# Optimization experiments

Measured on AMD Instinct MI355X. Metric: run time of the kernel, lower is better.

Reference implementation:

```python
import jax, jax.numpy as jnp
import numpy as np

E = 128          # embedding_dim
H = 128          # decoder_hidden_dim
N = 200000       # number of candidate nodes


def setup_inputs() -> dict:
    key = jax.random.key(0)
    k0, k1, k2, k3, k4, k5 = jax.random.split(key, 6)
    return {
        "current_node_emb": jax.random.normal(k0, (1, E), jnp.float32),
        "context_emb": jax.random.normal(k1, (1, E), jnp.float32),
        "candidate_node_embs": jax.random.normal(k2, (N, E), jnp.float32),
        "Wq": jax.random.normal(k3, (H, 2 * E), jnp.float32) * 0.05,  # nn.Linear(2E->H, bias=False) weight
        "Wk": jax.random.normal(k4, (H, E), jnp.float32) * 0.05,      # nn.Linear(E->H, bias=False) weight
        "mask": jax.random.randint(k5, (1, N), 0, 2, jnp.int32),
    }


def reference(current_node_emb, context_emb, candidate_node_embs, Wq, Wk, mask):
    # combined_input = cat([current, context], dim=1) -> [1, 2E]
    combined = jnp.concatenate([current_node_emb, context_emb], axis=1)
    query = combined @ Wq.T                      # [1, H]
    keys = candidate_node_embs @ Wk.T            # [N, H]
    attn_scores = query @ keys.T                 # [1, N]
    masked = jnp.where(mask == 0, -jnp.inf, attn_scores)
    probs = jax.nn.softmax(masked, axis=1)       # [1, N]

    n = probs.shape[1]
    k = min(50, max(1, int(0.5 * n)))            # static Python int -> jit-friendly
    top_probs, _ = jax.lax.top_k(probs, k)       # [1, k]
    threshold = top_probs[:, -1:]                # [1, 1]
    top_mask = probs >= threshold
    filtered = probs * top_mask
    filtered = filtered / (jnp.sum(filtered, axis=1, keepdims=True) + 1e-10)

    log_probs_all = jnp.log(filtered + 1e-10)    # [1, N]
    # Categorical(filtered): true-zero probability outside top-k
    logits = jnp.where(filtered > 0, jnp.log(filtered), -jnp.inf)
    action_idx = jax.random.categorical(jax.random.key(42), logits, axis=1)  # [1]
    log_prob_action = jnp.take_along_axis(logits, action_idx[:, None], axis=1)[:, 0]  # [1]
    return (log_probs_all, log_prob_action, action_idx)
```

## Files before the change

### kernel.cpp

```cpp
#include <hip/hip_runtime.h>
#include <math.h>


#define CAP 4096
#define NEG_INF (-__builtin_inff())

__device__ __forceinline__ unsigned int f2ord(float f){
  unsigned int b = __float_as_uint(f);
  return (b & 0x80000000u) ? ~b : (b | 0x80000000u);
}
__device__ __forceinline__ unsigned int rotl32(unsigned int x, int d){
  return (x << d) | (x >> (32 - d));
}

__device__ float gumbel_from_idx(unsigned int idx){
  unsigned int x0 = 0u, x1 = idx;
  const unsigned int ks0 = 0u, ks1 = 42u;
  const unsigned int ks2 = 0u ^ 42u ^ 0x1BD11BDAu;
  x0 += ks0; x1 += ks1;
#define TF_RND(r) { x0 += x1; x1 = rotl32(x1, (r)); x1 ^= x0; }
  TF_RND(13) TF_RND(15) TF_RND(26) TF_RND(6)
  x0 += ks1; x1 += ks2 + 1u;
  TF_RND(17) TF_RND(29) TF_RND(16) TF_RND(24)
  x0 += ks2; x1 += ks0 + 2u;
  TF_RND(13) TF_RND(15) TF_RND(26) TF_RND(6)
  x0 += ks0; x1 += ks1 + 3u;
  TF_RND(17) TF_RND(29) TF_RND(16) TF_RND(24)
  x0 += ks1; x1 += ks2 + 4u;
  TF_RND(13) TF_RND(15) TF_RND(26) TF_RND(6)
  x0 += ks2; x1 += ks0 + 5u;
#undef TF_RND
  unsigned int bits = x0 ^ x1;
  unsigned int fb = (bits >> 9) | 0x3f800000u;
  float f = __uint_as_float(fb) - 1.0f;
  float u = (f < 1.17549435e-38f) ? 1.17549435e-38f : f;
  return -logf(-logf(u));
}

__global__ void k_prep(const float* __restrict__ cur, const float* __restrict__ ctx,
                       const float* __restrict__ Wq, const float* __restrict__ Wk,
                       float* __restrict__ v, unsigned int* __restrict__ hist,
                       unsigned int* __restrict__ scal_u){
  __shared__ float comb[256];
  __shared__ float q[128];
  int t = threadIdx.x;
  for (int k = t; k < 2048; k += 256) hist[k] = 0u;
  if (t < 16) scal_u[t] = 0u;
  comb[t] = (t < 128) ? cur[t] : ctx[t - 128];
  __syncthreads();
  if (t < 128){
    float acc = 0.f;
    const float* row = Wq + t * 256;
    for (int j = 0; j < 256; ++j) acc = fmaf(row[j], comb[j], acc);
    q[t] = acc;
  }
  __syncthreads();
  if (t < 128){
    float acc = 0.f;
    for (int h = 0; h < 128; ++h) acc = fmaf(q[h], Wk[h * 128 + t], acc);
    v[t] = acc;
  }
}

__global__ __launch_bounds__(256) void k_score(const float* __restrict__ cand,
    const int* __restrict__ mask, const float* __restrict__ v,
    float* __restrict__ scores, float* __restrict__ out, int N){
  const float NLOG = logf(1e-10f);
  int t = threadIdx.x;
  int lane = t & 63, wave = t >> 6;
  int hi = lane >> 5, hl = lane & 31;
  float4 v4 = ((const float4*)v)[hl];
  const float4* cp = (const float4*)cand;
  int base = (blockIdx.x * 4 + wave) * 16;
  float4 c[8];
  #pragma unroll
  for (int k = 0; k < 8; ++k){
    int r = base + 2 * k + hi;
    r = (r < N) ? r : (N - 1);
    c[k] = cp[(size_t)r * 32 + hl];
  }
  float p[8];
  #pragma unroll
  for (int k = 0; k < 8; ++k)
    p[k] = fmaf(c[k].x, v4.x, fmaf(c[k].y, v4.y, fmaf(c[k].z, v4.z, c[k].w * v4.w)));
  #pragma unroll
  for (int k = 0; k < 8; ++k){
    p[k] += __shfl_xor(p[k], 1, 64);
    p[k] += __shfl_xor(p[k], 2, 64);
    p[k] += __shfl_xor(p[k], 4, 64);
    p[k] += __shfl_xor(p[k], 8, 64);
    p[k] += __shfl_xor(p[k], 16, 64);
  }
  float sv = p[0];
  #pragma unroll
  for (int k = 1; k < 8; ++k) sv = (hl == k) ? p[k] : sv;
  if (hl < 8){
    int r = base + 2 * hl + hi;
    if (r < N) scores[r] = mask[r] ? sv : NEG_INF;
  }
  int rr = blockIdx.x * 64 + t;
  if (t < 64 && rr < N) out[rr] = NLOG;
}

__global__ __launch_bounds__(256) void k_hist(const float* __restrict__ scores,
    unsigned int* __restrict__ hist, unsigned int* __restrict__ scal_u,
    int N, int ktop){
  __shared__ unsigned int lhist[2048];
  __shared__ float wsum[4];
  __shared__ int is_last;
  int t = threadIdx.x;
  int lane = t & 63, wave = t >> 6;
  for (int k = t; k < 2048; k += 256) lhist[k] = 0u;
  __syncthreads();
  float ez = 0.f;
  int i0 = (blockIdx.x * 256 + t) * 4;
  if (i0 + 3 < N){
    float4 s4 = *(const float4*)(scores + i0);
    float ss[4] = {s4.x, s4.y, s4.z, s4.w};
    #pragma unroll
    for (int e = 0; e < 4; ++e){
      if (ss[e] > NEG_INF){
        atomicAdd(&lhist[f2ord(ss[e]) >> 21], 1u);
        ez += expf(ss[e]);
      }
    }
  } else {
    for (int e = 0; e < 4; ++e){
      int i = i0 + e;
      if (i < N){
        float s = scores[i];
        if (s > NEG_INF){ atomicAdd(&lhist[f2ord(s) >> 21], 1u); ez += expf(s); }
      }
    }
  }
  #pragma unroll
  for (int off = 32; off; off >>= 1) ez += __shfl_xor(ez, off, 64);
  if (lane == 0) wsum[wave] = ez;
  __syncthreads();
  for (int k = t; k < 2048; k += 256){
    unsigned int c = lhist[k];
    if (c) atomicAdd(&hist[k], c);
  }
  if (t == 0) atomicAdd((float*)scal_u + 3, wsum[0] + wsum[1] + wsum[2] + wsum[3]);
  __syncthreads();
  if (t == 0){
    __threadfence();
    unsigned int old = atomicAdd(&scal_u[6], 1u);
    is_last = (old == gridDim.x - 1u);
  }
  __syncthreads();
  if (!is_last) return;
  __threadfence();
  __shared__ unsigned int suf[256];
  __shared__ int csel_sh;
  unsigned int csum = 0;
  for (int k = 0; k < 8; ++k) csum += hist[t * 8 + k];
  suf[t] = csum;
  if (t == 0) csel_sh = -1;
  __syncthreads();
  for (int d = 1; d < 256; d <<= 1){
    unsigned int add = (t + d < 256) ? suf[t + d] : 0u;
    __syncthreads();
    suf[t] += add;
    __syncthreads();
  }
  unsigned int st = suf[t];
  unsigned int sn = (t < 255) ? suf[t + 1] : 0u;
  if (st >= (unsigned)ktop && sn < (unsigned)ktop) csel_sh = t;
  __syncthreads();
  if (t == 0){
    int b_sel = 0;
    if (csel_sh >= 0){
      int c = csel_sh;
      unsigned int cum = (c < 255) ? suf[c + 1] : 0u;
      for (int b = 8 * c + 7; b >= 8 * c; --b){
        cum += hist[b];
        if (cum >= (unsigned)ktop){ b_sel = b; break; }
      }
    }
    scal_u[1] = ((unsigned int)b_sel) << 21;
  }
}

__global__ __launch_bounds__(256) void k_gather(const float* __restrict__ scores,
    unsigned int* __restrict__ scal_u, unsigned int* __restrict__ buf_idx,
    float* __restrict__ buf_s, float* __restrict__ out, int N, int ktop){
  int t = threadIdx.x;
  unsigned int u_lo = scal_u[1];
  int i0 = (blockIdx.x * 256 + t) * 4;
  if (i0 + 3 < N){
    float4 s4 = *(const float4*)(scores + i0);
    float ss[4] = {s4.x, s4.y, s4.z, s4.w};
    #pragma unroll
    for (int e = 0; e < 4; ++e){
      float s = ss[e];
      if (s > NEG_INF && f2ord(s) >= u_lo){
        unsigned int pos = atomicAdd(&scal_u[0], 1u);
        if (pos < CAP){ buf_idx[pos] = (unsigned int)(i0 + e); buf_s[pos] = s; }
      }
    }
  } else {
    for (int e = 0; e < 4; ++e){
      int i = i0 + e;
      if (i < N){
        float s = scores[i];
        if (s > NEG_INF && f2ord(s) >= u_lo){
          unsigned int pos = atomicAdd(&scal_u[0], 1u);
          if (pos < CAP){ buf_idx[pos] = (unsigned int)i; buf_s[pos] = s; }
        }
      }
    }
  }
  __syncthreads();
  __shared__ int is_last;
  if (t == 0){
    __threadfence();
    unsigned int old = atomicAdd(&scal_u[7], 1u);
    is_last = (old == gridDim.x - 1u);
  }
  __syncthreads();
  if (!is_last) return;
  __threadfence();
  float* scal_f = (float*)scal_u;
  __shared__ float s_lds[CAP];
  __shared__ float thr_sh;
  __shared__ float wred[4];
  __shared__ float rv[4], rl[4];
  __shared__ unsigned int ri[4];
  int C = (int)scal_u[0]; if (C > CAP) C = CAP;
  for (int j = t; j < C; j += 256) s_lds[j] = buf_s[j];
  if (t == 0) thr_sh = NEG_INF;
  __syncthreads();
  if (C > ktop){
    for (int j = t; j < C; j += 256){
      float sj = s_lds[j];
      int g = 0, e = 0;
      for (int k2 = 0; k2 < C; ++k2){
        float sk = s_lds[k2];
        g += (sk > sj);
        e += (sk == sj);
      }
      if (g < ktop && g + e >= ktop) thr_sh = sj;
    }
  }
  __syncthreads();
  float s_thr = thr_sh;
  float Z = scal_f[3];
  float part = 0.f;
  for (int j = t; j < C; j += 256){
    float sj = s_lds[j];
    if (sj >= s_thr) part += expf(sj);
  }
  #pragma unroll
  for (int off = 32; off; off >>= 1) part += __shfl_xor(part, off, 64);
  int wave = t >> 6, lane = t & 63;
  if (lane == 0) wred[wave] = part;
  __syncthreads();
  float T = wred[0] + wred[1] + wred[2] + wred[3];
  float D = T + 1e-10f * Z;
  float lnD = logf(D);
  for (int j = t; j < C; j += 256){
    float sj = s_lds[j];
    if (sj >= s_thr) out[buf_idx[j]] = logf(expf(sj - lnD) + 1e-10f);
  }
  float bestv = NEG_INF, bestlogit = NEG_INF;
  unsigned int bestidx = 0xFFFFFFFFu;
  for (int j = t; j < C; j += 256){
    float sj = s_lds[j];
    if (sj >= s_thr){
      unsigned int idx = buf_idx[j];
      float logit = sj - lnD;
      float val = logit + gumbel_from_idx(idx);
      if (val > bestv || (val == bestv && idx < bestidx)){
        bestv = val; bestlogit = logit; bestidx = idx;
      }
    }
  }
  #pragma unroll
  for (int off = 32; off; off >>= 1){
    float ov = __shfl_xor(bestv, off, 64);
    float ol = __shfl_xor(bestlogit, off, 64);
    unsigned int oi = (unsigned int)__shfl_xor((int)bestidx, off, 64);
    if (ov > bestv || (ov == bestv && oi < bestidx)){
      bestv = ov; bestlogit = ol; bestidx = oi;
    }
  }
  if (lane == 0){ rv[wave] = bestv; rl[wave] = bestlogit; ri[wave] = bestidx; }
  __syncthreads();
  if (t == 0){
    for (int w = 1; w < 4; ++w){
      if (rv[w] > rv[0] || (rv[w] == rv[0] && ri[w] < ri[0])){
        rv[0] = rv[w]; rl[0] = rl[w]; ri[0] = ri[w];
      }
    }
    out[N] = rl[0];
    out[N + 1] = (float)ri[0];
  }
}

extern "C" void kernel_launch(void* const* d_in, const int* in_sizes, int n_in,
                              void* d_out, int out_size, void* d_ws, size_t ws_size,
                              hipStream_t stream){
  const float* cur  = (const float*)d_in[0];
  const float* ctx  = (const float*)d_in[1];
  const float* cand = (const float*)d_in[2];
  const float* Wq   = (const float*)d_in[3];
  const float* Wk   = (const float*)d_in[4];
  const int*   mask = (const int*)d_in[5];
  int N = in_sizes[5];
  float* out = (float*)d_out;

  char* ws = (char*)d_ws;
  unsigned int* scal_u  = (unsigned int*)ws;
  unsigned int* hist    = (unsigned int*)(ws + 256);
  float*        v       = (float*)(ws + 256 + 8192);
  float*        scores  = (float*)(ws + 256 + 8192 + 512);
  char*         bufbase = ws + 256 + 8192 + 512 + 800000;
  unsigned int* buf_idx = (unsigned int*)bufbase;
  float*        buf_s   = (float*)(bufbase + CAP * 4);

  int ktop = N / 2; if (ktop < 1) ktop = 1; if (ktop > 50) ktop = 50;

  int g_score = (N + 63) / 64;
  int g_pass  = (N + 1023) / 1024;

  k_prep<<<1, 256, 0, stream>>>(cur, ctx, Wq, Wk, v, hist, scal_u);
  k_score<<<g_score, 256, 0, stream>>>(cand, mask, v, scores, out, N);
  k_hist<<<g_pass, 256, 0, stream>>>(scores, hist, scal_u, N, ktop);
  k_gather<<<g_pass, 256, 0, stream>>>(scores, scal_u, buf_idx, buf_s, out, N, ktop);
}
```

Measured before the change: 206.3 us.

## Fuse histogram and gather passes into one single-block finish kernel

The separate multi-block histogram and gather kernels, with their global atomics and last-block handoffs, are replaced by one 1024-thread block. That block builds a replicated LDS histogram, finds the top-k cutoff, compacts candidates into LDS and does the softmax and sampling. This removes one launch, the global counter and histogram atomics, and the workspace zeroing. The query/key projection in k_prep is rewritten with coalesced float4 loads and shuffle reductions, and the -inf output fill is vectorised. The risk is that a single CU now streams the whole score array twice, so that pass is limited by one CU's bandwidth and latency.

```diff
diff --git a/kernel.cpp b/kernel.cpp
--- a/kernel.cpp
+++ b/kernel.cpp
@@ -4,6 +4,8 @@
 
 #define CAP 4096
 #define NEG_INF (-__builtin_inff())
+#define HC 4
+#define HSTRIDE 2052
 
 __device__ __forceinline__ unsigned int f2ord(float f){
   unsigned int b = __float_as_uint(f);
@@ -37,29 +39,41 @@
   return -logf(-logf(u));
 }
 
-__global__ void k_prep(const float* __restrict__ cur, const float* __restrict__ ctx,
-                       const float* __restrict__ Wq, const float* __restrict__ Wk,
-                       float* __restrict__ v, unsigned int* __restrict__ hist,
-                       unsigned int* __restrict__ scal_u){
-  __shared__ float comb[256];
+__global__ __launch_bounds__(256) void k_prep(const float* __restrict__ cur,
+    const float* __restrict__ ctx, const float* __restrict__ Wq,
+    const float* __restrict__ Wk, float* __restrict__ v){
   __shared__ float q[128];
+  __shared__ float vpart[256];
   int t = threadIdx.x;
-  for (int k = t; k < 2048; k += 256) hist[k] = 0u;
-  if (t < 16) scal_u[t] = 0u;
-  comb[t] = (t < 128) ? cur[t] : ctx[t - 128];
-  __syncthreads();
-  if (t < 128){
-    float acc = 0.f;
-    const float* row = Wq + t * 256;
-    for (int j = 0; j < 256; ++j) acc = fmaf(row[j], comb[j], acc);
-    q[t] = acc;
-  }
-  __syncthreads();
-  if (t < 128){
-    float acc = 0.f;
-    for (int h = 0; h < 128; ++h) acc = fmaf(q[h], Wk[h * 128 + t], acc);
-    v[t] = acc;
-  }
+  int lane = t & 63, wave = t >> 6;
+  int hl = lane & 31, hi = lane >> 5;
+  float4 cb0 = ((const float4*)cur)[hl];
+  float4 cb1 = ((const float4*)ctx)[hl];
+  const float4* Wq4 = (const float4*)Wq;
+  #pragma unroll 4
+  for (int i = 0; i < 16; ++i){
+    int row = wave * 32 + 2 * i + hi;
+    float4 w0 = Wq4[row * 64 + hl];
+    float4 w1 = Wq4[row * 64 + 32 + hl];
+    float d = fmaf(w0.x, cb0.x, fmaf(w0.y, cb0.y, fmaf(w0.z, cb0.z, w0.w * cb0.w)));
+    d = fmaf(w1.x, cb1.x, fmaf(w1.y, cb1.y, fmaf(w1.z, cb1.z, fmaf(w1.w, cb1.w, d))));
+    d += __shfl_xor(d, 1, 64);
+    d += __shfl_xor(d, 2, 64);
+    d += __shfl_xor(d, 4, 64);
+    d += __shfl_xor(d, 8, 64);
+    d += __shfl_xor(d, 16, 64);
+    if (hl == 0) q[row] = d;
+  }
+  __syncthreads();
+  int col = t & 127, half = t >> 7;
+  const float* wkp = Wk + half * 64 * 128 + col;
+  const float* qp  = q + half * 64;
+  float acc = 0.f;
+  #pragma unroll 8
+  for (int h = 0; h < 64; ++h) acc = fmaf(qp[h], wkp[h * 128], acc);
+  vpart[t] = acc;
+  __syncthreads();
+  if (t < 128) v[t] = vpart[t] + vpart[t + 128];
 }
 
 __global__ __launch_bounds__(256) void k_score(const float* __restrict__ cand,
@@ -98,75 +112,93 @@
     int r = base + 2 * hl + hi;
     if (r < N) scores[r] = mask[r] ? sv : NEG_INF;
   }
-  int rr = blockIdx.x * 64 + t;
-  if (t < 64 && rr < N) out[rr] = NLOG;
-}
-
-__global__ __launch_bounds__(256) void k_hist(const float* __restrict__ scores,
-    unsigned int* __restrict__ hist, unsigned int* __restrict__ scal_u,
-    int N, int ktop){
-  __shared__ unsigned int lhist[2048];
-  __shared__ float wsum[4];
-  __shared__ int is_last;
+  if (t < 16){
+    int o4 = blockIdx.x * 16 + t;
+    if (o4 * 4 + 3 < N){
+      ((float4*)out)[o4] = make_float4(NLOG, NLOG, NLOG, NLOG);
+    } else {
+      #pragma unroll
+      for (int e = 0; e < 4; ++e){ int i = o4 * 4 + e; if (i < N) out[i] = NLOG; }
+    }
+  }
+}
+
+__global__ __launch_bounds__(1024) void k_finish(const float* __restrict__ scores,
+    float* __restrict__ out, int N, int ktop){
+  __shared__ unsigned int lh[HC * HSTRIDE];
+  __shared__ unsigned int htot[2048];
+  __shared__ unsigned int suf[256];
+  __shared__ float wred[16];
+  __shared__ float rv[16], rl[16];
+  __shared__ unsigned int ri[16];
+  __shared__ float zsh, thr_sh, lnD_sh;
+  __shared__ unsigned int u_lo_sh;
+  __shared__ int csel_sh, pos_sh, C_sh;
+  float* s_lds = (float*)lh;
+  unsigned int* i_lds = lh + CAP;
+
   int t = threadIdx.x;
   int lane = t & 63, wave = t >> 6;
-  for (int k = t; k < 2048; k += 256) lhist[k] = 0u;
-  __syncthreads();
+  unsigned int mycopy = (unsigned int)(t & (HC - 1)) * HSTRIDE;
+
+  for (int k = t; k < HC * HSTRIDE; k += 1024) lh[k] = 0u;
+  if (t == 0) pos_sh = 0;
+  __syncthreads();
+
   float ez = 0.f;
-  int i0 = (blockIdx.x * 256 + t) * 4;
-  if (i0 + 3 < N){
-    float4 s4 = *(const float4*)(scores + i0);
-    float ss[4] = {s4.x, s4.y, s4.z, s4.w};
+  const float4* sp4 = (const float4*)scores;
+  int nf = N >> 2;
+  const float4 SENT = make_float4(NEG_INF, NEG_INF, NEG_INF, NEG_INF);
+#define HVISIT(s_) { float sx = (s_); if (sx > NEG_INF){ \
+    atomicAdd(&lh[mycopy + (f2ord(sx) >> 21)], 1u); ez += expf(sx); } }
+  for (int f = t; f < nf; f += 4096){
+    float4 c0 = sp4[f];
+    float4 c1 = (f + 1024 < nf) ? sp4[f + 1024] : SENT;
+    float4 c2 = (f + 2048 < nf) ? sp4[f + 2048] : SENT;
+    float4 c3 = (f + 3072 < nf) ? sp4[f + 3072] : SENT;
+    HVISIT(c0.x) HVISIT(c0.y) HVISIT(c0.z) HVISIT(c0.w)
+    HVISIT(c1.x) HVISIT(c1.y) HVISIT(c1.z) HVISIT(c1.w)
+    HVISIT(c2.x) HVISIT(c2.y) HVISIT(c2.z) HVISIT(c2.w)
+    HVISIT(c3.x) HVISIT(c3.y) HVISIT(c3.z) HVISIT(c3.w)
+  }
+  for (int i = (nf << 2) + t; i < N; i += 1024) HVISIT(scores[i])
+#undef HVISIT
+  #pragma unroll
+  for (int off = 32; off; off >>= 1) ez += __shfl_xor(ez, off, 64);
+  if (lane == 0) wred[wave] = ez;
+  __syncthreads();
+  if (t == 0){
+    float z = 0.f;
+    for (int w = 0; w < 16; ++w) z += wred[w];
+    zsh = z; csel_sh = -1;
+  }
+  for (int k = t; k < 2048; k += 1024){
+    unsigned int c = 0;
     #pragma unroll
-    for (int e = 0; e < 4; ++e){
-      if (ss[e] > NEG_INF){
-        atomicAdd(&lhist[f2ord(ss[e]) >> 21], 1u);
-        ez += expf(ss[e]);
-      }
-    }
-  } else {
-    for (int e = 0; e < 4; ++e){
-      int i = i0 + e;
-      if (i < N){
-        float s = scores[i];
-        if (s > NEG_INF){ atomicAdd(&lhist[f2ord(s) >> 21], 1u); ez += expf(s); }
-      }
-    }
-  }
-  #pragma unroll
-  for (int off = 32; off; off >>= 1) ez += __shfl_xor(ez, off, 64);
-  if (lane == 0) wsum[wave] = ez;
-  __syncthreads();
-  for (int k = t; k < 2048; k += 256){
-    unsigned int c = lhist[k];
-    if (c) atomicAdd(&hist[k], c);
-  }
-  if (t == 0) atomicAdd((float*)scal_u + 3, wsum[0] + wsum[1] + wsum[2] + wsum[3]);
-  __syncthreads();
-  if (t == 0){
-    __threadfence();
-    unsigned int old = atomicAdd(&scal_u[6], 1u);
-    is_last = (old == gridDim.x - 1u);
-  }
-  __syncthreads();
-  if (!is_last) return;
-  __threadfence();
-  __shared__ unsigned int suf[256];
-  __shared__ int csel_sh;
-  unsigned int csum = 0;
-  for (int k = 0; k < 8; ++k) csum += hist[t * 8 + k];
-  suf[t] = csum;
-  if (t == 0) csel_sh = -1;
+    for (int cc = 0; cc < HC; ++cc) c += lh[cc * HSTRIDE + k];
+    htot[k] = c;
+  }
+  __syncthreads();
+
+  if (t < 256){
+    unsigned int csum = 0;
+    #pragma unroll
+    for (int k = 0; k < 8; ++k) csum += htot[t * 8 + k];
+    suf[t] = csum;
+  }
   __syncthreads();
   for (int d = 1; d < 256; d <<= 1){
-    unsigned int add = (t + d < 256) ? suf[t + d] : 0u;
+    unsigned int add = 0u;
+    if (t < 256 && t + d < 256) add = suf[t + d];
     __syncthreads();
-    suf[t] += add;
+    if (t < 256) suf[t] += add;
     __syncthreads();
   }
-  unsigned int st = suf[t];
-  unsigned int sn = (t < 255) ? suf[t + 1] : 0u;
-  if (st >= (unsigned)ktop && sn < (unsigned)ktop) csel_sh = t;
+  if (t < 256){
+    unsigned int st = suf[t];
+    unsigned int sn = (t < 255) ? suf[t + 1] : 0u;
+    if (st >= (unsigned)ktop && sn < (unsigned)ktop) csel_sh = t;
+  }
   __syncthreads();
   if (t == 0){
     int b_sel = 0;
@@ -174,65 +206,41 @@
       int c = csel_sh;
       unsigned int cum = (c < 255) ? suf[c + 1] : 0u;
       for (int b = 8 * c + 7; b >= 8 * c; --b){
-        cum += hist[b];
+        cum += htot[b];
         if (cum >= (unsigned)ktop){ b_sel = b; break; }
       }
     }
-    scal_u[1] = ((unsigned int)b_sel) << 21;
-  }
-}
-
-__global__ __launch_bounds__(256) void k_gather(const float* __restrict__ scores,
-    unsigned int* __restrict__ scal_u, unsigned int* __restrict__ buf_idx,
-    float* __restrict__ buf_s, float* __restrict__ out, int N, int ktop){
-  int t = threadIdx.x;
-  unsigned int u_lo = scal_u[1];
-  int i0 = (blockIdx.x * 256 + t) * 4;
-  if (i0 + 3 < N){
-    float4 s4 = *(const float4*)(scores + i0);
-    float ss[4] = {s4.x, s4.y, s4.z, s4.w};
-    #pragma unroll
-    for (int e = 0; e < 4; ++e){
-      float s = ss[e];
-      if (s > NEG_INF && f2ord(s) >= u_lo){
-        unsigned int pos = atomicAdd(&scal_u[0], 1u);
-        if (pos < CAP){ buf_idx[pos] = (unsigned int)(i0 + e); buf_s[pos] = s; }
-      }
-    }
-  } else {
-    for (int e = 0; e < 4; ++e){
-      int i = i0 + e;
-      if (i < N){
-        float s = scores[i];
-        if (s > NEG_INF && f2ord(s) >= u_lo){
-          unsigned int pos = atomicAdd(&scal_u[0], 1u);
-          if (pos < CAP){ buf_idx[pos] = (unsigned int)i; buf_s[pos] = s; }
-        }
-      }
-    }
-  }
-  __syncthreads();
-  __shared__ int is_last;
-  if (t == 0){
-    __threadfence();
-    unsigned int old = atomicAdd(&scal_u[7], 1u);
-    is_last = (old == gridDim.x - 1u);
-  }
-  __syncthreads();
-  if (!is_last) return;
-  __threadfence();
-  float* scal_f = (float*)scal_u;
-  __shared__ float s_lds[CAP];
-  __shared__ float thr_sh;
-  __shared__ float wred[4];
-  __shared__ float rv[4], rl[4];
-  __shared__ unsigned int ri[4];
-  int C = (int)scal_u[0]; if (C > CAP) C = CAP;
-  for (int j = t; j < C; j += 256) s_lds[j] = buf_s[j];
-  if (t == 0) thr_sh = NEG_INF;
-  __syncthreads();
+    u_lo_sh = ((unsigned int)b_sel) << 21;
+  }
+  __syncthreads();
+
+  unsigned int u_lo = u_lo_sh;
+#define GVISIT(s_, i_) { float sx = (s_); if (sx > NEG_INF && f2ord(sx) >= u_lo){ \
+    int p = atomicAdd(&pos_sh, 1); \
+    if (p < CAP){ s_lds[p] = sx; i_lds[p] = (unsigned int)(i_); } } }
+  for (int f = t; f < nf; f += 4096){
+    float4 c0 = sp4[f];
+    float4 c1 = (f + 1024 < nf) ? sp4[f + 1024] : SENT;
+    float4 c2 = (f + 2048 < nf) ? sp4[f + 2048] : SENT;
+    float4 c3 = (f + 3072 < nf) ? sp4[f + 3072] : SENT;
+    GVISIT(c0.x, 4*f)          GVISIT(c0.y, 4*f+1)
+    GVISIT(c0.z, 4*f+2)        GVISIT(c0.w, 4*f+3)
+    GVISIT(c1.x, 4*(f+1024))   GVISIT(c1.y, 4*(f+1024)+1)
+    GVISIT(c1.z, 4*(f+1024)+2) GVISIT(c1.w, 4*(f+1024)+3)
+    GVISIT(c2.x, 4*(f+2048))   GVISIT(c2.y, 4*(f+2048)+1)
+    GVISIT(c2.z, 4*(f+2048)+2) GVISIT(c2.w, 4*(f+2048)+3)
+    GVISIT(c3.x, 4*(f+3072))   GVISIT(c3.y, 4*(f+3072)+1)
+    GVISIT(c3.z, 4*(f+3072)+2) GVISIT(c3.w, 4*(f+3072)+3)
+  }
+  for (int i = (nf << 2) + t; i < N; i += 1024) GVISIT(scores[i], i)
+#undef GVISIT
+  __syncthreads();
+  if (t == 0){ C_sh = (pos_sh > CAP) ? CAP : pos_sh; thr_sh = NEG_INF; }
+  __syncthreads();
+  int C = C_sh;
+
   if (C > ktop){
-    for (int j = t; j < C; j += 256){
+    for (int j = t; j < C; j += 1024){
       float sj = s_lds[j];
       int g = 0, e = 0;
       for (int k2 = 0; k2 < C; ++k2){
@@ -245,30 +253,32 @@
   }
   __syncthreads();
   float s_thr = thr_sh;
-  float Z = scal_f[3];
   float part = 0.f;
-  for (int j = t; j < C; j += 256){
+  for (int j = t; j < C; j += 1024){
     float sj = s_lds[j];
     if (sj >= s_thr) part += expf(sj);
   }
   #pragma unroll
   for (int off = 32; off; off >>= 1) part += __shfl_xor(part, off, 64);
-  int wave = t >> 6, lane = t & 63;
   if (lane == 0) wred[wave] = part;
   __syncthreads();
-  float T = wred[0] + wred[1] + wred[2] + wred[3];
-  float D = T + 1e-10f * Z;
-  float lnD = logf(D);
-  for (int j = t; j < C; j += 256){
+  if (t == 0){
+    float T = 0.f;
+    for (int w = 0; w < 16; ++w) T += wred[w];
+    lnD_sh = logf(T + 1e-10f * zsh);
+  }
+  __syncthreads();
+  float lnD = lnD_sh;
+  for (int j = t; j < C; j += 1024){
     float sj = s_lds[j];
-    if (sj >= s_thr) out[buf_idx[j]] = logf(expf(sj - lnD) + 1e-10f);
+    if (sj >= s_thr) out[i_lds[j]] = logf(expf(sj - lnD) + 1e-10f);
   }
   float bestv = NEG_INF, bestlogit = NEG_INF;
   unsigned int bestidx = 0xFFFFFFFFu;
-  for (int j = t; j < C; j += 256){
+  for (int j = t; j < C; j += 1024){
     float sj = s_lds[j];
     if (sj >= s_thr){
-      unsigned int idx = buf_idx[j];
+      unsigned int idx = i_lds[j];
       float logit = sj - lnD;
       float val = logit + gumbel_from_idx(idx);
       if (val > bestv || (val == bestv && idx < bestidx)){
@@ -288,7 +298,7 @@
   if (lane == 0){ rv[wave] = bestv; rl[wave] = bestlogit; ri[wave] = bestidx; }
   __syncthreads();
   if (t == 0){
-    for (int w = 1; w < 4; ++w){
+    for (int w = 1; w < 16; ++w){
       if (rv[w] > rv[0] || (rv[w] == rv[0] && ri[w] < ri[0])){
         rv[0] = rv[w]; rl[0] = rl[w]; ri[0] = ri[w];
       }
@@ -311,21 +321,13 @@
   float* out = (float*)d_out;
 
   char* ws = (char*)d_ws;
-  unsigned int* scal_u  = (unsigned int*)ws;
-  unsigned int* hist    = (unsigned int*)(ws + 256);
-  float*        v       = (float*)(ws + 256 + 8192);
-  float*        scores  = (float*)(ws + 256 + 8192 + 512);
-  char*         bufbase = ws + 256 + 8192 + 512 + 800000;
-  unsigned int* buf_idx = (unsigned int*)bufbase;
-  float*        buf_s   = (float*)(bufbase + CAP * 4);
+  float* v      = (float*)ws;
+  float* scores = (float*)(ws + 512);
 
   int ktop = N / 2; if (ktop < 1) ktop = 1; if (ktop > 50) ktop = 50;
-
   int g_score = (N + 63) / 64;
-  int g_pass  = (N + 1023) / 1024;
-
-  k_prep<<<1, 256, 0, stream>>>(cur, ctx, Wq, Wk, v, hist, scal_u);
+
+  k_prep<<<1, 256, 0, stream>>>(cur, ctx, Wq, Wk, v);
   k_score<<<g_score, 256, 0, stream>>>(cand, mask, v, scores, out, N);
-  k_hist<<<g_pass, 256, 0, stream>>>(scores, hist, scal_u, N, ktop);
-  k_gather<<<g_pass, 256, 0, stream>>>(scores, scal_u, buf_idx, buf_s, out, N, ktop);
-}
+  k_finish<<<1, 1024, 0, stream>>>(scores, out, N, ktop);
+}
```

Result: slower. 261.5 us (+26.7%).
